# Kernel optimization log

Measured on AMD Instinct MI355X. Metric: run time of the kernel, lower is better.

The kernel has to match this reference:

```python
import jax, jax.numpy as jnp
import numpy as np

# model hyperparameters (from init_kwargs)
N_IN = 2048
NN = 512
BATCH = 64
DT, TAU_M, TAU_X = 0.05, 10.0, 2.0
ALPHA = 1.0 - DT / TAU_M   # membrane decay
BETA = 1.0 - DT / TAU_X    # lateral-trace decay
V_TH = 2.0


def _loo_idx(nn):
    # leave-one-out gather indices: idx[j, n] = j if j < n else j + 1
    j = np.arange(nn - 1)[:, None]
    n = np.arange(nn)[None, :]
    return jnp.asarray(j + (j >= n))  # (nn-1, nn) int


def setup_inputs() -> dict:
    key = jax.random.key(0)
    k1, k2, k3, k4 = jax.random.split(key, 4)
    x = jax.random.uniform(k1, (BATCH, N_IN, NN), dtype=jnp.float32)      # per-neuron external input
    v = jax.random.normal(k2, (BATCH, NN), dtype=jnp.float32)             # membrane state
    z = jnp.zeros((BATCH, NN), dtype=jnp.float32)                         # previous spikes
    z_out = jax.random.uniform(k3, (BATCH, NN), dtype=jnp.float32)        # lateral spike trace
    w = jax.random.normal(k4, (N_IN + NN - 1, NN), dtype=jnp.float32) / np.sqrt(N_IN)
    return {"x": x, "v": v, "z": z, "z_out": z_out, "w": w}


def reference(x, v, z, z_out, w):
    # update lateral trace: z_out = beta * z_out + z (z detached in original)
    z_out_new = BETA * z_out + z
    # leave-one-out lateral input: z_loo[b, j, n] = z_out_new[b, j + (j >= n)]
    idx = _loo_idx(NN)
    z_loo = z_out_new[:, idx]  # (B, NN-1, NN)
    # membrane drive: sum_k x_tot[b,k,n] * w[k,n], where x_tot = cat([x, z_loo], dim=1)
    drive = (jnp.einsum('bkn,kn->bn', x, w[:N_IN])
             + jnp.einsum('bjn,jn->bn', z_loo, w[N_IN:]))
    v_new = ALPHA * v + drive - V_TH * z
    # thresholding nonlinearity -> output spikes
    z_new = (v_new - V_TH > 0).astype(v.dtype)
    return v_new, z_new, z_out_new
```

## Files before the change

kernel.cpp:

```cpp
#include <hip/hip_runtime.h>

#define BATCH 64
#define N_IN  2048
#define NN    512
#define NCH   64
#define G     4
#define KR    4
#define ALPHA 0.995f
#define BETA  0.975f
#define V_TH  2.0f

__global__ __launch_bounds__(1024, 8)
void k1_drive1(const float* __restrict__ x,
               const float* __restrict__ w,
               float4* __restrict__ ws)
{
    const int nc  = blockIdx.x;
    const int b0  = blockIdx.y * G;
    const int kr  = blockIdx.z;
    const int tid = threadIdx.x;
    const int nl  = tid & 15;
    const int kk  = tid >> 4;
    const int wid  = tid >> 6;
    const int lane = tid & 63;

    const float4* __restrict__ x4 = (const float4*)x;
    const float4* __restrict__ w4 = (const float4*)w;
    const int    c4    = nc * 16 + nl;
    const int    kbase = kr * 512 + kk;

    size_t xoff[G];
#pragma unroll
    for (int g = 0; g < G; ++g)
        xoff[g] = ((size_t)(b0 + g) * N_IN + kbase) * 128 + c4;
    size_t woff = (size_t)kbase * 128 + c4;

    float4 acc[G];
#pragma unroll
    for (int g = 0; g < G; ++g) acc[g] = make_float4(0.f, 0.f, 0.f, 0.f);

    const size_t kstep = (size_t)64 * 128;
#pragma unroll 1
    for (int i = 0; i < 8; ++i) {
        float4 xv[G];
#pragma unroll
        for (int g = 0; g < G; ++g) xv[g] = x4[xoff[g]];
        const float4 wv = w4[woff];
#pragma unroll
        for (int g = 0; g < G; ++g) {
            acc[g].x += xv[g].x * wv.x;
            acc[g].y += xv[g].y * wv.y;
            acc[g].z += xv[g].z * wv.z;
            acc[g].w += xv[g].w * wv.w;
        }
#pragma unroll
        for (int g = 0; g < G; ++g) xoff[g] += kstep;
        woff += kstep;
    }

#pragma unroll
    for (int off = 32; off >= 16; off >>= 1) {
#pragma unroll
        for (int g = 0; g < G; ++g) {
            acc[g].x += __shfl_down(acc[g].x, off);
            acc[g].y += __shfl_down(acc[g].y, off);
            acc[g].z += __shfl_down(acc[g].z, off);
            acc[g].w += __shfl_down(acc[g].w, off);
        }
    }

    __shared__ float4 wpart[16][G][16];
    if (lane < 16) {
#pragma unroll
        for (int g = 0; g < G; ++g) wpart[wid][g][lane] = acc[g];
    }
    __syncthreads();

    if (tid < 64) {
        const int g = tid >> 4, c = tid & 15;
        float4 s = wpart[0][g][c];
#pragma unroll
        for (int ww = 1; ww < 16; ++ww) {
            const float4 o = wpart[ww][g][c];
            s.x += o.x; s.y += o.y; s.z += o.z; s.w += o.w;
        }
        ws[((size_t)kr * BATCH + b0 + g) * 128 + nc * 16 + c] = s;
    }
}

__global__ __launch_bounds__(1024)
void k2_finish(const float* __restrict__ v,
               const float* __restrict__ z,
               const float* __restrict__ z_out,
               const float* __restrict__ w,
               const float* __restrict__ ws,
               float* __restrict__ out)
{
    const int nc  = blockIdx.x;
    const int b   = blockIdx.y;
    const int nb  = nc * 64;
    const int tid = threadIdx.x;

    __shared__ float zlds[NN];
    __shared__ float r2[1024];

    if (tid < NN)
        zlds[tid] = BETA * z_out[b * NN + tid] + z[b * NN + tid];
    __syncthreads();

    const int n_loc = tid & 63;
    const int n     = nb + n_loc;
    const int jg    = tid >> 6;
    float d2 = 0.f;
#pragma unroll 4
    for (int j = jg; j < NN - 1; j += 16)
        d2 += zlds[j + (j >= n)] * w[(size_t)(N_IN + j) * NN + n];
    r2[tid] = d2;
    __syncthreads();

    if (tid < 64) {
        float d1 = 0.f;
#pragma unroll
        for (int kr = 0; kr < KR; ++kr)
            d1 += ws[((size_t)kr * BATCH + b) * NN + n];
        float d2s = 0.f;
#pragma unroll
        for (int g = 0; g < 16; ++g) d2s += r2[g * 64 + n_loc];
        const float vv    = v[b * NN + n];
        const float zz    = z[b * NN + n];
        const float v_new = ALPHA * vv + d1 + d2s - V_TH * zz;
        out[b * NN + n]                  = v_new;
        out[BATCH * NN + b * NN + n]     = (v_new - V_TH > 0.f) ? 1.f : 0.f;
        out[2 * BATCH * NN + b * NN + n] = zlds[n];
    }
}

extern "C" void kernel_launch(void* const* d_in, const int* in_sizes, int n_in,
                              void* d_out, int out_size, void* d_ws, size_t ws_size,
                              hipStream_t stream) {
    (void)in_sizes; (void)n_in; (void)out_size; (void)ws_size;
    const float* x     = (const float*)d_in[0];
    const float* v     = (const float*)d_in[1];
    const float* z     = (const float*)d_in[2];
    const float* z_out = (const float*)d_in[3];
    const float* w     = (const float*)d_in[4];
    float* out = (float*)d_out;
    float* wsf = (float*)d_ws;

    dim3 g1(8, BATCH / G, KR);
    k1_drive1<<<g1, 1024, 0, stream>>>(x, w, (float4*)wsf);
    dim3 g2(8, BATCH);
    k2_finish<<<g2, 1024, 0, stream>>>(v, z, z_out, w, wsf, out);
}
```

Before: 53.66 us.

## Restructure drive kernel to span all columns per block with 32-way K split

The first kernel now has each block cover all 512 neuron columns (128 float4 lanes) for a 64-row K slice, which gives 32 K-partitions. It reduces them through a shared-memory tree instead of wavefront shuffles. The finish kernel is templated on the partition count and sums 32 partials per output. A fallback keeps the old 4-way layout when the workspace is too small. Each block's loads become contiguous full rows of x and w, but the partial-sum traffic grows and a larger workspace is required.

```diff
diff --git a/kernel.cpp b/kernel.cpp
--- a/kernel.cpp
+++ b/kernel.cpp
@@ -3,9 +3,7 @@
 #define BATCH 64
 #define N_IN  2048
 #define NN    512
-#define NCH   64
 #define G     4
-#define KR    4
 #define ALPHA 0.995f
 #define BETA  0.975f
 #define V_TH  2.0f
@@ -14,6 +12,68 @@
 void k1_drive1(const float* __restrict__ x,
                const float* __restrict__ w,
                float4* __restrict__ ws)
+{
+    const int kr  = blockIdx.x;
+    const int b0  = blockIdx.y * G;
+    const int tid = threadIdx.x;
+    const int c4  = tid & 127;
+    const int kl  = tid >> 7;
+
+    const float4* __restrict__ x4 = (const float4*)x;
+    const float4* __restrict__ w4 = (const float4*)w;
+    const int k0 = kr * 64 + kl;
+
+    size_t xoff[G];
+#pragma unroll
+    for (int g = 0; g < G; ++g)
+        xoff[g] = ((size_t)(b0 + g) * N_IN + k0) * 128 + c4;
+    size_t woff = (size_t)k0 * 128 + c4;
+    const size_t kstep = 8 * 128;
+
+    float4 acc[G];
+#pragma unroll
+    for (int g = 0; g < G; ++g) acc[g] = make_float4(0.f, 0.f, 0.f, 0.f);
+
+#pragma unroll 2
+    for (int i = 0; i < 8; ++i) {
+        float4 xv[G];
+#pragma unroll
+        for (int g = 0; g < G; ++g) xv[g] = x4[xoff[g]];
+        const float4 wv = w4[woff];
+#pragma unroll
+        for (int g = 0; g < G; ++g) {
+            acc[g].x += xv[g].x * wv.x;
+            acc[g].y += xv[g].y * wv.y;
+            acc[g].z += xv[g].z * wv.z;
+            acc[g].w += xv[g].w * wv.w;
+        }
+#pragma unroll
+        for (int g = 0; g < G; ++g) xoff[g] += kstep;
+        woff += kstep;
+    }
+
+    __shared__ float4 red[G][8][128];
+#pragma unroll
+    for (int g = 0; g < G; ++g) red[g][kl][c4] = acc[g];
+    __syncthreads();
+
+    if (tid < 512) {
+        const int g = tid >> 7, c = tid & 127;
+        float4 s = red[g][0][c];
+#pragma unroll
+        for (int l = 1; l < 8; ++l) {
+            const float4 o = red[g][l][c];
+            s.x += o.x; s.y += o.y; s.z += o.z; s.w += o.w;
+        }
+        ws[((size_t)kr * BATCH + b0 + g) * 128 + c] = s;
+    }
+}
+
+#define KRF 4
+__global__ __launch_bounds__(1024, 8)
+void k1_fallback(const float* __restrict__ x,
+                 const float* __restrict__ w,
+                 float4* __restrict__ ws)
 {
     const int nc  = blockIdx.x;
     const int b0  = blockIdx.y * G;
@@ -26,8 +86,8 @@
 
     const float4* __restrict__ x4 = (const float4*)x;
     const float4* __restrict__ w4 = (const float4*)w;
-    const int    c4    = nc * 16 + nl;
-    const int    kbase = kr * 512 + kk;
+    const int c4    = nc * 16 + nl;
+    const int kbase = kr * 512 + kk;
 
     size_t xoff[G];
 #pragma unroll
@@ -40,7 +100,7 @@
     for (int g = 0; g < G; ++g) acc[g] = make_float4(0.f, 0.f, 0.f, 0.f);
 
     const size_t kstep = (size_t)64 * 128;
-#pragma unroll 1
+#pragma unroll 2
     for (int i = 0; i < 8; ++i) {
         float4 xv[G];
 #pragma unroll
@@ -88,6 +148,7 @@
     }
 }
 
+template <int KRV>
 __global__ __launch_bounds__(1024)
 void k2_finish(const float* __restrict__ v,
                const float* __restrict__ z,
@@ -121,7 +182,7 @@
     if (tid < 64) {
         float d1 = 0.f;
 #pragma unroll
-        for (int kr = 0; kr < KR; ++kr)
+        for (int kr = 0; kr < KRV; ++kr)
             d1 += ws[((size_t)kr * BATCH + b) * NN + n];
         float d2s = 0.f;
 #pragma unroll
@@ -138,7 +199,7 @@
 extern "C" void kernel_launch(void* const* d_in, const int* in_sizes, int n_in,
                               void* d_out, int out_size, void* d_ws, size_t ws_size,
                               hipStream_t stream) {
-    (void)in_sizes; (void)n_in; (void)out_size; (void)ws_size;
+    (void)in_sizes; (void)n_in; (void)out_size;
     const float* x     = (const float*)d_in[0];
     const float* v     = (const float*)d_in[1];
     const float* z     = (const float*)d_in[2];
@@ -147,8 +208,16 @@
     float* out = (float*)d_out;
     float* wsf = (float*)d_ws;
 
-    dim3 g1(8, BATCH / G, KR);
-    k1_drive1<<<g1, 1024, 0, stream>>>(x, w, (float4*)wsf);
-    dim3 g2(8, BATCH);
-    k2_finish<<<g2, 1024, 0, stream>>>(v, z, z_out, w, wsf, out);
-}
+    const size_t need32 = (size_t)32 * BATCH * NN * sizeof(float);
+    if (ws_size >= need32) {
+        dim3 g1(32, BATCH / G);
+        k1_drive1<<<g1, 1024, 0, stream>>>(x, w, (float4*)wsf);
+        dim3 g2(8, BATCH);
+        k2_finish<32><<<g2, 1024, 0, stream>>>(v, z, z_out, w, wsf, out);
+    } else {
+        dim3 g1(8, BATCH / G, KRF);
+        k1_fallback<<<g1, 1024, 0, stream>>>(x, w, (float4*)wsf);
+        dim3 g2(8, BATCH);
+        k2_finish<KRF><<<g2, 1024, 0, stream>>>(v, z, z_out, w, wsf, out);
+    }
+}
```

After: 53.49 us. Within noise of the previous version (-0.3%).
